# Kernel tuning notes

Measured on AMD Instinct MI355X. Metric: run time of the kernel, lower is better.

Reference implementation:

```python
import jax, jax.numpy as jnp
import numpy as np

EPS = 1e-8  # PoissonNLLLoss default eps

def _pair_loss(inp, tgt):
    # Poisson NLL (log_input=False, full=True), summed over detector dim D,
    # for every (hypothesis i, measurement j) pair WITHOUT materializing [N,M,D]:
    # loss_ij = sum_d inp[i,d] - sum_d tgt[j,d]*log(inp[i,d]+eps) + sum_d stirling(tgt[j,d])
    log_in = jnp.log(inp + EPS)                         # [N,D]
    s_in = jnp.sum(inp, axis=1)                         # [N]
    cross = jnp.einsum('id,jd->ij', log_in, tgt)        # [N,M]
    t_safe = jnp.where(tgt > 1, tgt, 1.0)
    stirling = jnp.where(
        tgt > 1,
        tgt * jnp.log(t_safe) - tgt + 0.5 * jnp.log(2.0 * jnp.pi * t_safe),
        0.0,
    )
    s_st = jnp.sum(stirling, axis=1)                    # [M]
    return s_in[:, None] - cross + s_st[None, :]        # [N,M]

def setup_inputs() -> dict:
    key = jax.random.key(0)
    k1, k2 = jax.random.split(key)
    N, M, D = 10000, 10000, 180
    # photon-count-like positive values; scale so target>1 hits Stirling branch
    inp = jax.random.uniform(k1, (N, D), dtype=jnp.float32) * 100.0
    tgt = jax.random.uniform(k2, (M, D), dtype=jnp.float32) * 100.0
    return {"input": inp, "target": tgt}

def reference(input, target):
    L = _pair_loss(input, target)          # [N,M]
    loss_v = jnp.min(L, axis=1)            # [N]
    match = jnp.argmin(L, axis=1)          # [N] int
    loss = jnp.mean(loss_v)
    return (loss, match)
```

## Files before the change

kernel.cpp:

```cpp
#include <hip/hip_runtime.h>
#include <math.h>

#define EPSF 1e-8f

typedef _Float16 f16x8 __attribute__((ext_vector_type(8)));
typedef float f32x4 __attribute__((ext_vector_type(4)));

#define GLOAD_LDS16(g, l)                                                      \
  __builtin_amdgcn_global_load_lds(                                            \
      (const __attribute__((address_space(1))) unsigned int*)(g),              \
      (__attribute__((address_space(3))) unsigned int*)(l), 16, 0, 0)

#define WAITV(n) asm volatile("s_waitcnt vmcnt(" #n ")" ::: "memory")
#define BAR() __builtin_amdgcn_s_barrier()
#define SBAR0() __builtin_amdgcn_sched_barrier(0)

__device__ __forceinline__ unsigned int ord_from_float(float f) {
  unsigned int u = __float_as_uint(f);
  return (u & 0x80000000u) ? ~u : (u | 0x80000000u);
}

__device__ __forceinline__ float float_from_ord(unsigned int o) {
  return (o & 0x80000000u) ? __uint_as_float(o & 0x7fffffffu)
                           : __uint_as_float(~o);
}

__device__ __forceinline__ unsigned long long shfl_xor_u64(unsigned long long x, int m) {
  int lo = __shfl_xor((int)(unsigned int)(x & 0xffffffffull), m, 64);
  int hi = __shfl_xor((int)(unsigned int)(x >> 32), m, 64);
  return ((unsigned long long)(unsigned int)hi << 32) | (unsigned int)lo;
}

__global__ __launch_bounds__(64) void prep_A_kernel(
    const float* __restrict__ inp, _Float16* __restrict__ Acat,
    float* __restrict__ s_in, unsigned long long* __restrict__ packed,
    int N, int D, int DP, int KPA) {
  int r = blockIdx.x;
  _Float16* row = Acat + (size_t)r * KPA;
  float s = 0.f;
  for (int d = threadIdx.x; d < DP; d += 64) {
    float lg = 0.f;
    if (r < N && d < D) {
      float x = inp[(size_t)r * D + d];
      s += x;
      lg = logf(x + EPSF);
    }
    _Float16 h = (_Float16)lg;
    _Float16 l = (_Float16)(lg - (float)h);
    row[d] = h;
    row[DP + d] = h;
    row[2 * DP + d] = l;
  }
  for (int d = threadIdx.x; d < KPA - 3 * DP; d += 64) row[3 * DP + d] = (_Float16)0.f;
  #pragma unroll
  for (int m = 1; m < 64; m <<= 1) s += __shfl_xor(s, m, 64);
  if (threadIdx.x == 0 && r < N) {
    s_in[r] = s;
    packed[r] = ~0ull;
  }
}

__global__ __launch_bounds__(64) void prep_B_kernel(
    const float* __restrict__ tgt, _Float16* __restrict__ Bcat,
    float* __restrict__ s_st, int M, int D, int DP, int KPA) {
  int r = blockIdx.x;
  _Float16* row = Bcat + (size_t)r * KPA;
  float s = 0.f;
  for (int d = threadIdx.x; d < DP; d += 64) {
    float x = 0.f;
    if (r < M && d < D) {
      x = tgt[(size_t)r * D + d];
      if (x > 1.0f)
        s += x * logf(x) - x + 0.5f * logf(6.283185307179586f * x);
    }
    _Float16 h = (_Float16)x;
    _Float16 l = (_Float16)(x - (float)h);
    row[d] = h;
    row[DP + d] = l;
    row[2 * DP + d] = h;
  }
  for (int d = threadIdx.x; d < KPA - 3 * DP; d += 64) row[3 * DP + d] = (_Float16)0.f;
  #pragma unroll
  for (int m = 1; m < 64; m <<= 1) s += __shfl_xor(s, m, 64);
  if (threadIdx.x == 0 && r < M) s_st[r] = s;
}

#define BT 256
#define SUBH 8192
#define SUB(d_, o_, k_) (((((d_) << 1) | (o_)) << 1) | (k_))

__global__ __launch_bounds__(512, 2) void mfma_pair_min_kernel(
    const _Float16* __restrict__ Acat, const _Float16* __restrict__ Bcat,
    const float* __restrict__ s_st, unsigned long long* __restrict__ packed,
    int N, int M, int KPA, int gx) {
  extern __shared__ __align__(16) _Float16 smem[];
  const int t = threadIdx.x;
  const int lane = t & 63;
  const int wid = t >> 6;
  const int wr = wid >> 2;
  const int wc = wid & 3;

  const int nwg = gridDim.x;
  const int q8 = nwg >> 3;
  const int xcd = blockIdx.x & 7;
  const int i8 = blockIdx.x >> 3;
  int brow, bcol;
  if (q8 % gx == 0) {
    int bh = q8 / gx;
    brow = xcd * bh + i8 % bh;
    bcol = i8 / bh;
  } else {
    int wg = xcd * q8 + i8;
    brow = wg / gx;
    bcol = wg % gx;
  }
  const int row0 = brow * BT;
  const int col0 = bcol * BT;

  const int srow = lane >> 2;
  const int gs = (lane & 3) ^ ((lane >> 3) & 3);
  const _Float16* const aSt = Acat + (size_t)(row0 + wid * 16 + srow) * KPA + gs * 8;
  const _Float16* const bSt = Bcat + (size_t)(col0 + wid * 16 + srow) * KPA + gs * 8;

#define STG(DD_, O_, H_, KT_)                                                  \
  do {                                                                         \
    const _Float16* gb_ = ((O_) ? bSt : aSt) + (size_t)(H_) * 128 * KPA +      \
                          (size_t)(KT_) * 64;                                  \
    _Float16* lb_ = smem + ((H_) * 128 + wid * 16) * 32;                       \
    GLOAD_LDS16(gb_, lb_ + SUB(DD_, O_, 0) * SUBH);                            \
    GLOAD_LDS16(gb_ + 32, lb_ + SUB(DD_, O_, 1) * SUBH);                       \
  } while (0)

  const int rl = lane & 15;
  const int qq = lane >> 4;
  const int sa = qq ^ ((rl >> 1) & 3);

#define LDA(SET_, D_, QR_)                                                     \
  do {                                                                         \
    _Pragma("unroll") for (int mm = 0; mm < 4; ++mm)                           \
      _Pragma("unroll") for (int kh = 0; kh < 2; ++kh)                         \
        SET_[mm][kh] = *(const f16x8*)(smem + SUB(D_, 0, kh) * SUBH +          \
            (wr * 128 + (QR_) * 64 + mm * 16 + rl) * 32 + sa * 8);             \
  } while (0)

#define LDB(SET_, D_, QC_)                                                     \
  do {                                                                         \
    _Pragma("unroll") for (int nn = 0; nn < 2; ++nn)                           \
      _Pragma("unroll") for (int kh = 0; kh < 2; ++kh)                         \
        SET_[nn][kh] = *(const f16x8*)(smem + SUB(D_, 1, kh) * SUBH +          \
            (wc * 64 + (QC_) * 32 + nn * 16 + rl) * 32 + sa * 8);              \
  } while (0)

  f32x4 acc[8][4] = {};
  f16x8 Aq0[4][2], Aq1[4][2], Bq0[2][2], Bq1[2][2];

#define MMQ(A_, B_, QR_, QC_)                                                  \
  do {                                                                         \
    __builtin_amdgcn_s_setprio(1);                                             \
    _Pragma("unroll") for (int mm = 0; mm < 4; ++mm)                           \
      _Pragma("unroll") for (int nn = 0; nn < 2; ++nn)                         \
        _Pragma("unroll") for (int kh = 0; kh < 2; ++kh)                       \
          acc[(QR_) * 4 + mm][(QC_) * 2 + nn] =                                \
              __builtin_amdgcn_mfma_f32_16x16x32_f16(                          \
                  A_[mm][kh], B_[nn][kh], acc[(QR_) * 4 + mm][(QC_) * 2 + nn], \
                  0, 0, 0);                                                    \
    __builtin_amdgcn_s_setprio(0);                                             \
  } while (0)

  const int NTILE = KPA >> 6;

  STG(0, 0, 0, 0); STG(0, 0, 1, 0); STG(0, 1, 0, 0); STG(0, 1, 1, 0);
  STG(1, 0, 0, 1);
  WAITV(2);
  BAR();
  LDA(Aq0, 0, 0);

  for (int T = 0; T < NTILE; ++T) {
    const int d = T & 1, nd = d ^ 1;
    const bool last = (T == NTILE - 1);
    if (last) { WAITV(0); } else { WAITV(2); }
    LDB(Bq0, d, 0);
    if (!last) STG(nd, 0, 1, T + 1);
    SBAR0();
    BAR();
    MMQ(Aq0, Bq0, 0, 0);
    BAR();
    LDB(Bq1, d, 1);
    if (!last) STG(nd, 1, 0, T + 1);
    SBAR0();
    BAR();
    MMQ(Aq0, Bq1, 0, 1);
    BAR();
    LDA(Aq1, d, 1);
    if (!last) STG(nd, 1, 1, T + 1);
    SBAR0();
    BAR();
    MMQ(Aq1, Bq1, 1, 1);
    BAR();
    if (!last) {
      WAITV(4);
      LDA(Aq0, nd, 0);
      if (T < NTILE - 2) STG(d, 0, 0, T + 2);
    }
    SBAR0();
    BAR();
    MMQ(Aq1, Bq0, 1, 0);
    BAR();
  }

#undef STG
#undef LDA
#undef LDB
#undef MMQ

  float stv[4];
  #pragma unroll
  for (int n = 0; n < 4; ++n) {
    int gj = col0 + wc * 64 + n * 16 + rl;
    stv[n] = (gj < M) ? s_st[gj] : __builtin_inff();
  }
  #pragma unroll
  for (int m = 0; m < 8; ++m) {
    #pragma unroll
    for (int g = 0; g < 4; ++g) {
      int grow = row0 + wr * 128 + m * 16 + qq * 4 + g;
      unsigned long long bst = ~0ull;
      #pragma unroll
      for (int n = 0; n < 4; ++n) {
        int gj = col0 + wc * 64 + n * 16 + rl;
        float val = stv[n] - acc[m][n][g];
        unsigned long long p =
            ((unsigned long long)ord_from_float(val) << 32) | (unsigned int)gj;
        if (p < bst) bst = p;
      }
      #pragma unroll
      for (int mm = 1; mm < 16; mm <<= 1) {
        unsigned long long o = shfl_xor_u64(bst, mm);
        if (o < bst) bst = o;
      }
      if (rl == 0 && grow < N) atomicMin(&packed[grow], bst);
    }
  }
}


__global__ __launch_bounds__(256) void finalize_kernel(
    const unsigned long long* __restrict__ packed,
    const float* __restrict__ s_in, float* __restrict__ out, int N) {
  __shared__ double sh[256];
  double s = 0.0;
  for (int i = threadIdx.x; i < N; i += 256) {
    unsigned long long p = packed[i];
    float val = float_from_ord((unsigned int)(p >> 32));
    out[1 + i] = (float)(unsigned int)(p & 0xffffffffull);
    s += (double)(s_in[i] + val);
  }
  sh[threadIdx.x] = s;
  __syncthreads();
  for (int off = 128; off > 0; off >>= 1) {
    if (threadIdx.x < off) sh[threadIdx.x] += sh[threadIdx.x + off];
    __syncthreads();
  }
  if (threadIdx.x == 0) out[0] = (float)(sh[0] / N);
}

extern "C" void kernel_launch(void* const* d_in, const int* in_sizes, int n_in,
                              void* d_out, int out_size, void* d_ws, size_t ws_size,
                              hipStream_t stream) {
  const float* inp = (const float*)d_in[0];
  const float* tgt = (const float*)d_in[1];
  float* out = (float*)d_out;

  int N = out_size - 1;
  int D = in_sizes[0] / N;
  int M = in_sizes[1] / D;

  int Npad = ((N + BT - 1) / BT) * BT;
  int Mpad = ((M + BT - 1) / BT) * BT;
  int DP = ((D + 31) / 32) * 32;
  int KPA = ((3 * DP + 63) / 64) * 64;

  char* ws = (char*)d_ws;
  size_t off = 0;
  float* s_in = (float*)(ws + off); off += (size_t)N * 4;
  float* s_st = (float*)(ws + off); off += (size_t)M * 4;
  off = (off + 15) & ~(size_t)15;
  unsigned long long* packed = (unsigned long long*)(ws + off); off += (size_t)N * 8;
  off = (off + 15) & ~(size_t)15;
  _Float16* Acat = (_Float16*)(ws + off); off += (size_t)Npad * KPA * 2;
  _Float16* Bcat = (_Float16*)(ws + off); off += (size_t)Mpad * KPA * 2;

  prep_A_kernel<<<Npad, 64, 0, stream>>>(inp, Acat, s_in, packed, N, D, DP, KPA);
  prep_B_kernel<<<Mpad, 64, 0, stream>>>(tgt, Bcat, s_st, M, D, DP, KPA);

  const int ldsBytes = 8 * SUBH * 2;
  hipFuncSetAttribute((const void*)mfma_pair_min_kernel,
                      hipFuncAttributeMaxDynamicSharedMemorySize, ldsBytes);

  int gx = Mpad / BT, gy = Npad / BT;
  mfma_pair_min_kernel<<<gx * gy, 512, ldsBytes, stream>>>(Acat, Bcat, s_st,
                                                           packed, N, M, KPA, gx);

  finalize_kernel<<<1, 256, 0, stream>>>(packed, s_in, out, N);
}
```

Baseline: 209.9 us.

## Restructure MFMA main loop into unrolled double-tile pipeline with snake quadrant order

Rewrites the GEMM K-loop into a manually unrolled two-tile-per-iteration schedule that reorders the quadrant MFMAs in a snake pattern (00,10,11,01) so that fragments in registers are reused across consecutive quadrants. It also adjusts the staging of global-to-LDS loads and adds explicit lgkmcnt waits. K padding is forced to an odd number of 64-wide tiles so the unrolled loop plus epilogue covers all tiles. This may add padded K work, since KPA can grow by one tile.

```diff
diff --git a/kernel.cpp b/kernel.cpp
--- a/kernel.cpp
+++ b/kernel.cpp
@@ -12,6 +12,7 @@
       (__attribute__((address_space(3))) unsigned int*)(l), 16, 0, 0)
 
 #define WAITV(n) asm volatile("s_waitcnt vmcnt(" #n ")" ::: "memory")
+#define LGKM(n) asm volatile("s_waitcnt lgkmcnt(" #n ")" ::: "memory")
 #define BAR() __builtin_amdgcn_s_barrier()
 #define SBAR0() __builtin_amdgcn_sched_barrier(0)
 
@@ -167,51 +168,68 @@
     __builtin_amdgcn_s_setprio(0);                                             \
   } while (0)
 
+#define OPEN() do { SBAR0(); BAR(); LGKM(0); SBAR0(); } while (0)
+#define CLOSE() BAR()
+
   const int NTILE = KPA >> 6;
+  const int LITERS = (NTILE - 3) >> 1;
 
   STG(0, 0, 0, 0); STG(0, 0, 1, 0); STG(0, 1, 0, 0); STG(0, 1, 1, 0);
-  STG(1, 0, 0, 1);
-  WAITV(2);
+  STG(1, 0, 0, 1); STG(1, 0, 1, 1);
+  WAITV(4);
+  SBAR0();
   BAR();
-  LDA(Aq0, 0, 0);
-
-  for (int T = 0; T < NTILE; ++T) {
-    const int d = T & 1, nd = d ^ 1;
-    const bool last = (T == NTILE - 1);
-    if (last) { WAITV(0); } else { WAITV(2); }
-    LDB(Bq0, d, 0);
-    if (!last) STG(nd, 0, 1, T + 1);
-    SBAR0();
-    BAR();
-    MMQ(Aq0, Bq0, 0, 0);
-    BAR();
-    LDB(Bq1, d, 1);
-    if (!last) STG(nd, 1, 0, T + 1);
-    SBAR0();
-    BAR();
-    MMQ(Aq0, Bq1, 0, 1);
-    BAR();
-    LDA(Aq1, d, 1);
-    if (!last) STG(nd, 1, 1, T + 1);
-    SBAR0();
-    BAR();
-    MMQ(Aq1, Bq1, 1, 1);
-    BAR();
-    if (!last) {
+
+  for (int i = 0; i <= LITERS; ++i) {
+    const int Tb = 2 * i;
+    const bool red = (i == LITERS);
+    LDA(Aq0, 0, 0); LDB(Bq0, 0, 0);
+    STG(1, 1, 0, Tb + 1);
+    LGKM(8);
+    OPEN(); MMQ(Aq0, Bq0, 0, 0); CLOSE();
+    LDA(Aq1, 0, 1);
+    STG(1, 1, 1, Tb + 1);
+    OPEN(); MMQ(Aq1, Bq0, 1, 0); CLOSE();
+    LDB(Bq1, 0, 1);
+    STG(0, 0, 0, Tb + 2);
+    OPEN(); MMQ(Aq1, Bq1, 1, 1); CLOSE();
+    STG(0, 0, 1, Tb + 2);
+    WAITV(4);
+    OPEN(); MMQ(Aq0, Bq1, 0, 1); CLOSE();
+    LDA(Aq0, 1, 0); LDB(Bq0, 1, 0);
+    STG(0, 1, 0, Tb + 2);
+    LGKM(8);
+    OPEN(); MMQ(Aq0, Bq0, 0, 0); CLOSE();
+    LDA(Aq1, 1, 1);
+    STG(0, 1, 1, Tb + 2);
+    OPEN(); MMQ(Aq1, Bq0, 1, 0); CLOSE();
+    LDB(Bq1, 1, 1);
+    if (!red) STG(1, 0, 0, Tb + 3);
+    OPEN(); MMQ(Aq1, Bq1, 1, 1); CLOSE();
+    if (!red) {
+      STG(1, 0, 1, Tb + 3);
       WAITV(4);
-      LDA(Aq0, nd, 0);
-      if (T < NTILE - 2) STG(d, 0, 0, T + 2);
+    } else {
+      WAITV(0);
     }
-    SBAR0();
-    BAR();
-    MMQ(Aq1, Bq0, 1, 0);
-    BAR();
-  }
+    OPEN(); MMQ(Aq0, Bq1, 0, 1); CLOSE();
+  }
+
+  LDA(Aq0, 0, 0); LDB(Bq0, 0, 0);
+  LGKM(8);
+  OPEN(); MMQ(Aq0, Bq0, 0, 0); CLOSE();
+  LDA(Aq1, 0, 1);
+  OPEN(); MMQ(Aq1, Bq0, 1, 0); CLOSE();
+  LDB(Bq1, 0, 1);
+  OPEN(); MMQ(Aq1, Bq1, 1, 1); CLOSE();
+  OPEN(); MMQ(Aq0, Bq1, 0, 1);
 
 #undef STG
 #undef LDA
 #undef LDB
 #undef MMQ
+#undef OPEN
+#undef CLOSE
 
   float stv[4];
   #pragma unroll
@@ -278,7 +296,9 @@
   int Npad = ((N + BT - 1) / BT) * BT;
   int Mpad = ((M + BT - 1) / BT) * BT;
   int DP = ((D + 31) / 32) * 32;
-  int KPA = ((3 * DP + 63) / 64) * 64;
+  int TT = (3 * DP + 63) / 64;
+  if ((TT & 1) == 0) ++TT;
+  int KPA = TT * 64;
 
   char* ws = (char*)d_ws;
   size_t off = 0;
```

After: 211.2 us. Within noise of the previous version (+0.6%).
